# Optimization experiments

Hardware: AMD Instinct MI355X
Metric: run time of the kernel (lower is better)

The kernel has to match this reference:

```python
import jax, jax.numpy as jnp
import numpy as np

C = 128      # channels
ALPHA = 0.5
B, LX, LY = 8, 128, 1024


def setup_inputs() -> dict:
    key = jax.random.key(0)
    ks = jax.random.split(key, 10)
    s = 1.0 / np.sqrt(C)
    sh = 1.0 / np.sqrt(C // 2)
    return {
        "x": jax.random.normal(ks[0], (B, C, LX), dtype=jnp.float32),
        "y": jax.random.normal(ks[1], (B, C, LY), dtype=jnp.float32),
        "W_drug": jax.random.uniform(ks[2], (C, C), jnp.float32, -s, s),
        "b_drug": jax.random.uniform(ks[3], (C,), jnp.float32, -s, s),
        "W_prot": jax.random.uniform(ks[4], (C, C), jnp.float32, -s, s),
        "b_prot": jax.random.uniform(ks[5], (C,), jnp.float32, -s, s),
        "W_down": jax.random.uniform(ks[6], (C, C // 2), jnp.float32, -s, s),
        "b_down": jax.random.uniform(ks[7], (C // 2,), jnp.float32, -s, s),
        "W_up": jax.random.uniform(ks[8], (C // 2, C), jnp.float32, -sh, sh),
        "b_up": jax.random.uniform(ks[9], (C,), jnp.float32, -sh, sh),
    }


def reference(x, y, W_drug, b_drug, W_prot, b_prot, W_down, b_down, W_up, b_up):
    # x: [B, C, Lx], y: [B, C, Ly]
    drug_att = jnp.einsum("bcl,cd->bld", x, W_drug) + b_drug      # [B, Lx, C]
    prot_att = jnp.einsum("bcl,cd->bld", y, W_prot) + b_prot      # [B, Ly, C]
    # broadcast-add -> [B, Lx, Ly, C]
    s = jax.nn.relu(drug_att[:, :, None, :] + prot_att[:, None, :, :])
    h = jax.nn.relu(jnp.einsum("bxyc,ch->bxyh", s, W_down) + b_down)  # [B,Lx,Ly,C/2]
    atten = jnp.einsum("bxyh,hc->bxyc", h, W_up) + b_up              # [B,Lx,Ly,C]
    comp = jnp.mean(atten, axis=2)   # [B, Lx, C]
    prot = jnp.mean(atten, axis=1)   # [B, Ly, C]
    comp_g = comp.transpose(0, 2, 1)  # [B, C, Lx]
    prot_g = prot.transpose(0, 2, 1)  # [B, C, Ly]
    comp_gate = jax.nn.sigmoid(comp_g) * jnp.tanh(comp_g)
    prot_gate = jax.nn.sigmoid(prot_g) * jnp.tanh(prot_g)
    drug_out = x * ALPHA + x * comp_gate
    prot_out = y * ALPHA + y * prot_gate
    return (drug_out, prot_out)
```

## Files before the change

kernel.cpp:

```cpp
#include <hip/hip_runtime.h>
#include <hip/hip_bf16.h>
#include <math.h>

#define B_  8
#define C_  128
#define CH_ 64
#define LX_ 128
#define LY_ 1024

typedef __attribute__((ext_vector_type(8)))  _Float16 half8;
typedef __attribute__((ext_vector_type(16))) float f32x16;

__global__ __launch_bounds__(128) void k1_att(
    const float* __restrict__ x, const float* __restrict__ y,
    const float* __restrict__ Wd, const float* __restrict__ bd,
    const float* __restrict__ Wp, const float* __restrict__ bp,
    const float* __restrict__ Wdown,
    _Float16* __restrict__ datt, _Float16* __restrict__ patt,
    _Float16* __restrict__ wdTh)
{
    const int blk = blockIdx.x;
    const int t = threadIdx.x;
    if (blk < 64) {
        int u = blk * 128 + t;
        wdTh[u] = (_Float16)Wdown[(u & 127) * CH_ + (u >> 7)];
    }
    const float* src; const float* W; const float* bias; _Float16* dst; int L;
    int b, l0;
    if (blk < 256) {
        int row0 = blk * 4; b = row0 >> 7; l0 = row0 & 127;
        src = x; W = Wd; bias = bd; dst = datt; L = LX_;
    } else {
        int row0 = (blk - 256) * 4; b = row0 >> 10; l0 = row0 & 1023;
        src = y; W = Wp; bias = bp; dst = patt; L = LY_;
    }
    __shared__ float col[4][128];
    {
        const float* sp = src + ((long)b * C_ + t) * L + l0;
        float4 v = *(const float4*)sp;
        col[0][t] = v.x; col[1][t] = v.y; col[2][t] = v.z; col[3][t] = v.w;
    }
    __syncthreads();
    float acc0 = bias[t], acc1 = acc0, acc2 = acc0, acc3 = acc0;
    #pragma unroll 8
    for (int c = 0; c < 128; ++c) {
        float w = W[c * 128 + t];
        float s0 = col[0][c], s1 = col[1][c], s2 = col[2][c], s3 = col[3][c];
        acc0 = fmaf(s0, w, acc0); acc1 = fmaf(s1, w, acc1);
        acc2 = fmaf(s2, w, acc2); acc3 = fmaf(s3, w, acc3);
    }
    _Float16* dp = dst + ((long)b * L + l0) * C_ + t;
    dp[0]      = (_Float16)acc0; dp[C_]     = (_Float16)acc1;
    dp[2 * C_] = (_Float16)acc2; dp[3 * C_] = (_Float16)acc3;
}

__global__ __launch_bounds__(256, 3) void k2_main(
    const _Float16* __restrict__ datt, const _Float16* __restrict__ patt,
    const _Float16* __restrict__ wdTh, const float* __restrict__ bdown,
    float* __restrict__ HxP, float* __restrict__ HyP)
{
    const int b     = blockIdx.x >> 2;
    const int lxblk = blockIdx.x & 3;
    const int lyblk = blockIdx.y;
    const int t   = threadIdx.x;
    const int w   = t >> 6;
    const int wk  = w >> 1;
    const int wl  = w & 1;
    const int l   = t & 63;
    const int h   = l >> 5;
    const int c32 = l & 31;

    __shared__ float compWp[32][2][66];
    __shared__ float protP[2][32][66];

    const _Float16* prow = patt + ((long)(b * LY_) + lyblk * 32 + c32) * C_;
    const _Float16* wrow = wdTh + (wk * 32 + c32) * C_;
    half8 pv[8], bf[8];
    #pragma unroll
    for (int kt = 0; kt < 8; ++kt) {
        pv[kt] = *(const half8*)(prow + kt * 16 + h * 8);
        bf[kt] = *(const half8*)(wrow + kt * 16 + h * 8);
    }
    const float bdr = bdown[wk * 32 + c32];

    const _Float16* dbase = datt + ((long)(b * LX_) + lxblk * 32) * C_;
    const half8 hz = {};
    float hy[16];
    #pragma unroll
    for (int r = 0; r < 16; ++r) hy[r] = 0.f;

    #pragma unroll 1
    for (int lxp = 0; lxp < 8; ++lxp) {
        const int lxa = wl * 16 + lxp * 2;
        const _Float16* da = dbase + lxa * C_ + h * 8;
        f32x16 accA = {}, accB = {};
        #pragma unroll
        for (int kt = 0; kt < 8; ++kt) {
            half8 dva = *(const half8*)(da + kt * 16);
            half8 dvb = *(const half8*)(da + C_ + kt * 16);
            half8 sa = __builtin_elementwise_max(dva + pv[kt], hz);
            half8 sb = __builtin_elementwise_max(dvb + pv[kt], hz);
            accA = __builtin_amdgcn_mfma_f32_32x32x16_f16(sa, bf[kt], accA, 0, 0, 0);
            accB = __builtin_amdgcn_mfma_f32_32x32x16_f16(sb, bf[kt], accB, 0, 0, 0);
        }
        float sA = 0.f, sB = 0.f;
        #pragma unroll
        for (int r = 0; r < 16; ++r) {
            float va = fmaxf(accA[r] + bdr, 0.f);
            float vb = fmaxf(accB[r] + bdr, 0.f);
            hy[r] += va + vb;
            sA += va; sB += vb;
        }
        compWp[lxa][h][wk * 32 + c32]     = sA;
        compWp[lxa + 1][h][wk * 32 + c32] = sB;
    }

    #pragma unroll
    for (int r = 0; r < 16; ++r) {
        int ly = (r & 3) + 8 * (r >> 2) + 4 * h;
        protP[wl][ly][wk * 32 + c32] = hy[r];
    }
    __syncthreads();

    {
        float* hxp = HxP + ((long)lyblk * (B_ * LX_) + b * LX_ + lxblk * 32) * 64;
        float* hyp = HyP + ((long)lxblk * (B_ * LY_) + b * LY_ + lyblk * 32) * 64;
        for (int u = t; u < 2048; u += 256) {
            int r = u >> 6, c = u & 63;
            hxp[u] = compWp[r][0][c] + compWp[r][1][c];
            hyp[u] = protP[0][r][c] + protP[1][r][c];
        }
    }
}

__global__ __launch_bounds__(256) void k3_gate(
    const float* __restrict__ HxP, const float* __restrict__ HyP,
    const float* __restrict__ wup, const float* __restrict__ bup,
    const float* __restrict__ x, const float* __restrict__ y,
    float* __restrict__ out)
{
    const int b = blockIdx.y;
    const int t = threadIdx.x;
    const float* part; const float* xin; float* outp; int L; float invN; int l0;
    int nq; long qstr;
    if (blockIdx.x < 4) {
        part = HxP; nq = 32; qstr = (long)B_ * LX_ * 64;
        xin = x; outp = out; L = LX_; invN = 1.f / 1024.f; l0 = blockIdx.x * 32;
    } else {
        part = HyP; nq = 4;  qstr = (long)B_ * LY_ * 64;
        xin = y; outp = out + (long)B_ * C_ * LX_; L = LY_; invN = 1.f / 128.f;
        l0 = (blockIdx.x - 4) * 32;
    }
    __shared__ float Ht[32][72];
    __shared__ float Wt[64][136];
    __shared__ float gg[32][133];

    const float* p0 = part + ((long)b * L + l0) * 64;
    for (int u = t; u < 2048; u += 256) {
        float a0 = 0.f, a1 = 0.f, a2 = 0.f, a3 = 0.f;
        #pragma unroll 4
        for (int q = 0; q < nq; q += 4) {
            a0 += p0[(long)q * qstr + u];
            a1 += p0[(long)(q + 1) * qstr + u];
            a2 += p0[(long)(q + 2) * qstr + u];
            a3 += p0[(long)(q + 3) * qstr + u];
        }
        Ht[u >> 6][u & 63] = (a0 + a1) + (a2 + a3);
    }
    #pragma unroll
    for (int i = 0; i < 8; ++i) {
        int idx = t + i * 256;
        int r = idx >> 5, c4 = (idx & 31) * 4;
        *(float4*)&Wt[r][c4] = *(const float4*)(wup + idx * 4);
    }
    __syncthreads();

    const int lrow = t >> 3, cg = (t & 7) * 4;
    float acc[4][4];
    #pragma unroll
    for (int jj = 0; jj < 4; ++jj)
        #pragma unroll
        for (int i = 0; i < 4; ++i) acc[jj][i] = 0.f;
    #pragma unroll 4
    for (int k = 0; k < 64; ++k) {
        float hv = Ht[lrow][k];
        #pragma unroll
        for (int jj = 0; jj < 4; ++jj) {
            float4 wv = *(const float4*)&Wt[k][cg + 32 * jj];
            acc[jj][0] = fmaf(hv, wv.x, acc[jj][0]);
            acc[jj][1] = fmaf(hv, wv.y, acc[jj][1]);
            acc[jj][2] = fmaf(hv, wv.z, acc[jj][2]);
            acc[jj][3] = fmaf(hv, wv.w, acc[jj][3]);
        }
    }
    #pragma unroll
    for (int jj = 0; jj < 4; ++jj)
        #pragma unroll
        for (int i = 0; i < 4; ++i) {
            int c = cg + 32 * jj + i;
            float v = fmaf(acc[jj][i], invN, bup[c]);
            float sg = 1.f / (1.f + expf(-v));
            gg[lrow][c] = sg * tanhf(v);
        }
    __syncthreads();
    for (int u = t; u < 4096; u += 256) {
        int c = u >> 5, li = u & 31;
        long idx = ((long)b * C_ + c) * L + l0 + li;
        outp[idx] = xin[idx] * (0.5f + gg[li][c]);
    }
}

extern "C" void kernel_launch(void* const* d_in, const int* in_sizes, int n_in,
                              void* d_out, int out_size, void* d_ws, size_t ws_size,
                              hipStream_t stream) {
    (void)in_sizes; (void)n_in; (void)out_size; (void)ws_size;
    const float* x     = (const float*)d_in[0];
    const float* y     = (const float*)d_in[1];
    const float* Wdrug = (const float*)d_in[2];
    const float* bdrug = (const float*)d_in[3];
    const float* Wprot = (const float*)d_in[4];
    const float* bprot = (const float*)d_in[5];
    const float* Wdown = (const float*)d_in[6];
    const float* bdown = (const float*)d_in[7];
    const float* Wup   = (const float*)d_in[8];
    const float* bup   = (const float*)d_in[9];
    float* out = (float*)d_out;
    char* ws = (char*)d_ws;

    _Float16* datt = (_Float16*)ws;
    _Float16* patt = (_Float16*)(ws + 262144);
    _Float16* wdTh = (_Float16*)(ws + 2359296);
    float*    HxP  = (float*)(ws + 2375680);
    float*    HyP  = (float*)(ws + 10764288);

    hipLaunchKernelGGL(k1_att, dim3(2304), dim3(128), 0, stream,
                       x, y, Wdrug, bdrug, Wprot, bprot, Wdown, datt, patt, wdTh);
    hipLaunchKernelGGL(k2_main, dim3(32, 32, 1), dim3(256), 0, stream,
                       datt, patt, wdTh, bdown, HxP, HyP);
    hipLaunchKernelGGL(k3_gate, dim3(36, 8), dim3(256), 0, stream,
                       HxP, HyP, Wup, bup, x, y, out);
}
```

Measured before the change: 71.32 us.

## Loop each k2 block over four ly tiles and prefetch next drug rows

The main kernel's grid shrinks from 32x32 to 32x8 blocks, and each block now walks four ly tiles in sequence, reloading the protein rows per tile and keeping the down-projection weights in registers throughout. Inside the lx loop, the next pair of drug rows is loaded into registers before the MFMA chain runs, so global-load latency overlaps compute. The comp partial sums are also split into four independent accumulators to shorten the dependency chain. In exchange the kernel uses more registers, so launch bounds drop to two blocks per SM. It also adds an extra barrier per tile, and the smaller grid gives fewer blocks to balance across the 256 CUs.

```diff
diff --git a/kernel.cpp b/kernel.cpp
--- a/kernel.cpp
+++ b/kernel.cpp
@@ -54,14 +54,13 @@
     dp[2 * C_] = (_Float16)acc2; dp[3 * C_] = (_Float16)acc3;
 }
 
-__global__ __launch_bounds__(256, 3) void k2_main(
+__global__ __launch_bounds__(256, 2) void k2_main(
     const _Float16* __restrict__ datt, const _Float16* __restrict__ patt,
     const _Float16* __restrict__ wdTh, const float* __restrict__ bdown,
     float* __restrict__ HxP, float* __restrict__ HyP)
 {
     const int b     = blockIdx.x >> 2;
     const int lxblk = blockIdx.x & 3;
-    const int lyblk = blockIdx.y;
     const int t   = threadIdx.x;
     const int w   = t >> 6;
     const int wk  = w >> 1;
@@ -73,63 +72,88 @@
     __shared__ float compWp[32][2][66];
     __shared__ float protP[2][32][66];
 
-    const _Float16* prow = patt + ((long)(b * LY_) + lyblk * 32 + c32) * C_;
-    const _Float16* wrow = wdTh + (wk * 32 + c32) * C_;
-    half8 pv[8], bf[8];
-    #pragma unroll
-    for (int kt = 0; kt < 8; ++kt) {
-        pv[kt] = *(const half8*)(prow + kt * 16 + h * 8);
-        bf[kt] = *(const half8*)(wrow + kt * 16 + h * 8);
-    }
+    const _Float16* wrow = wdTh + (wk * 32 + c32) * C_ + h * 8;
+    half8 bf[8];
+    #pragma unroll
+    for (int kt = 0; kt < 8; ++kt) bf[kt] = *(const half8*)(wrow + kt * 16);
     const float bdr = bdown[wk * 32 + c32];
-
-    const _Float16* dbase = datt + ((long)(b * LX_) + lxblk * 32) * C_;
+    const _Float16* dbase =
+        datt + ((long)(b * LX_) + lxblk * 32 + wl * 16) * C_ + h * 8;
     const half8 hz = {};
-    float hy[16];
-    #pragma unroll
-    for (int r = 0; r < 16; ++r) hy[r] = 0.f;
 
     #pragma unroll 1
-    for (int lxp = 0; lxp < 8; ++lxp) {
-        const int lxa = wl * 16 + lxp * 2;
-        const _Float16* da = dbase + lxa * C_ + h * 8;
-        f32x16 accA = {}, accB = {};
+    for (int tt = 0; tt < 4; ++tt) {
+        const int lyblk = blockIdx.y * 4 + tt;
+        const _Float16* prow =
+            patt + ((long)(b * LY_) + lyblk * 32 + c32) * C_ + h * 8;
+        half8 pv[8];
+        #pragma unroll
+        for (int kt = 0; kt < 8; ++kt) pv[kt] = *(const half8*)(prow + kt * 16);
+
+        float hy[16];
+        #pragma unroll
+        for (int r = 0; r < 16; ++r) hy[r] = 0.f;
+
+        half8 dva[8], dvb[8];
         #pragma unroll
         for (int kt = 0; kt < 8; ++kt) {
-            half8 dva = *(const half8*)(da + kt * 16);
-            half8 dvb = *(const half8*)(da + C_ + kt * 16);
-            half8 sa = __builtin_elementwise_max(dva + pv[kt], hz);
-            half8 sb = __builtin_elementwise_max(dvb + pv[kt], hz);
-            accA = __builtin_amdgcn_mfma_f32_32x32x16_f16(sa, bf[kt], accA, 0, 0, 0);
-            accB = __builtin_amdgcn_mfma_f32_32x32x16_f16(sb, bf[kt], accB, 0, 0, 0);
-        }
-        float sA = 0.f, sB = 0.f;
+            dva[kt] = *(const half8*)(dbase + kt * 16);
+            dvb[kt] = *(const half8*)(dbase + C_ + kt * 16);
+        }
+
+        #pragma unroll 1
+        for (int lxp = 0; lxp < 8; ++lxp) {
+            half8 sa[8], sb[8];
+            #pragma unroll
+            for (int kt = 0; kt < 8; ++kt) {
+                sa[kt] = __builtin_elementwise_max(dva[kt] + pv[kt], hz);
+                sb[kt] = __builtin_elementwise_max(dvb[kt] + pv[kt], hz);
+            }
+            if (lxp < 7) {
+                const _Float16* dn = dbase + (lxp * 2 + 2) * C_;
+                #pragma unroll
+                for (int kt = 0; kt < 8; ++kt) {
+                    dva[kt] = *(const half8*)(dn + kt * 16);
+                    dvb[kt] = *(const half8*)(dn + C_ + kt * 16);
+                }
+            }
+            f32x16 accA = {}, accB = {};
+            #pragma unroll
+            for (int kt = 0; kt < 8; ++kt) {
+                accA = __builtin_amdgcn_mfma_f32_32x32x16_f16(sa[kt], bf[kt], accA, 0, 0, 0);
+                accB = __builtin_amdgcn_mfma_f32_32x32x16_f16(sb[kt], bf[kt], accB, 0, 0, 0);
+            }
+            const int lxa = wl * 16 + lxp * 2;
+            float pa[4] = {0.f, 0.f, 0.f, 0.f}, pb[4] = {0.f, 0.f, 0.f, 0.f};
+            #pragma unroll
+            for (int r = 0; r < 16; ++r) {
+                float va = fmaxf(accA[r] + bdr, 0.f);
+                float vb = fmaxf(accB[r] + bdr, 0.f);
+                hy[r] += va + vb;
+                pa[r & 3] += va;
+                pb[r & 3] += vb;
+            }
+            compWp[lxa][h][wk * 32 + c32]     = (pa[0] + pa[1]) + (pa[2] + pa[3]);
+            compWp[lxa + 1][h][wk * 32 + c32] = (pb[0] + pb[1]) + (pb[2] + pb[3]);
+        }
+
         #pragma unroll
         for (int r = 0; r < 16; ++r) {
-            float va = fmaxf(accA[r] + bdr, 0.f);
-            float vb = fmaxf(accB[r] + bdr, 0.f);
-            hy[r] += va + vb;
-            sA += va; sB += vb;
-        }
-        compWp[lxa][h][wk * 32 + c32]     = sA;
-        compWp[lxa + 1][h][wk * 32 + c32] = sB;
-    }
-
-    #pragma unroll
-    for (int r = 0; r < 16; ++r) {
-        int ly = (r & 3) + 8 * (r >> 2) + 4 * h;
-        protP[wl][ly][wk * 32 + c32] = hy[r];
-    }
-    __syncthreads();
-
-    {
-        float* hxp = HxP + ((long)lyblk * (B_ * LX_) + b * LX_ + lxblk * 32) * 64;
-        float* hyp = HyP + ((long)lxblk * (B_ * LY_) + b * LY_ + lyblk * 32) * 64;
-        for (int u = t; u < 2048; u += 256) {
-            int r = u >> 6, c = u & 63;
-            hxp[u] = compWp[r][0][c] + compWp[r][1][c];
-            hyp[u] = protP[0][r][c] + protP[1][r][c];
-        }
+            int ly = (r & 3) + 8 * (r >> 2) + 4 * h;
+            protP[wl][ly][wk * 32 + c32] = hy[r];
+        }
+        __syncthreads();
+
+        {
+            float* hxp = HxP + ((long)lyblk * (B_ * LX_) + b * LX_ + lxblk * 32) * 64;
+            float* hyp = HyP + ((long)lxblk * (B_ * LY_) + b * LY_ + lyblk * 32) * 64;
+            for (int u = t; u < 2048; u += 256) {
+                int r = u >> 6, c = u & 63;
+                hxp[u] = compWp[r][0][c] + compWp[r][1][c];
+                hyp[u] = protP[0][r][c] + protP[1][r][c];
+            }
+        }
+        __syncthreads();
     }
 }
 
@@ -235,7 +259,7 @@
 
     hipLaunchKernelGGL(k1_att, dim3(2304), dim3(128), 0, stream,
                        x, y, Wdrug, bdrug, Wprot, bprot, Wdown, datt, patt, wdTh);
-    hipLaunchKernelGGL(k2_main, dim3(32, 32, 1), dim3(256), 0, stream,
+    hipLaunchKernelGGL(k2_main, dim3(32, 8), dim3(256), 0, stream,
                        datt, patt, wdTh, bdown, HxP, HyP);
     hipLaunchKernelGGL(k3_gate, dim3(36, 8), dim3(256), 0, stream,
                        HxP, HyP, Wup, bup, x, y, out);
```

Measured after the change: 79.06 us. +10.9%, slower.

## Split k2 warps over lx rows, compute both hidden halves per warp with prefetch

Applied to the files above, without the earlier changes.

Each of the four warps in k2_main now owns 8 lx rows and computes both 32-column halves of the hidden layer. This lets one relu'd activation tile feed two MFMAs, so the add/max work on the operand is halved. The next row's datt fragment is double-buffered in registers so its global loads overlap the current MFMAs. The cost is higher register pressure (two weight fragment sets, two hy accumulators, two data buffers), handled by lowering the occupancy hint from 3 to 2 blocks, plus a larger protP shared buffer reduced over four warps.

```diff
diff --git a/kernel.cpp b/kernel.cpp
--- a/kernel.cpp
+++ b/kernel.cpp
@@ -54,7 +54,7 @@
     dp[2 * C_] = (_Float16)acc2; dp[3 * C_] = (_Float16)acc3;
 }
 
-__global__ __launch_bounds__(256, 3) void k2_main(
+__global__ __launch_bounds__(256, 2) void k2_main(
     const _Float16* __restrict__ datt, const _Float16* __restrict__ patt,
     const _Float16* __restrict__ wdTh, const float* __restrict__ bdown,
     float* __restrict__ HxP, float* __restrict__ HyP)
@@ -64,61 +64,82 @@
     const int lyblk = blockIdx.y;
     const int t   = threadIdx.x;
     const int w   = t >> 6;
-    const int wk  = w >> 1;
-    const int wl  = w & 1;
     const int l   = t & 63;
     const int h   = l >> 5;
     const int c32 = l & 31;
 
     __shared__ float compWp[32][2][66];
-    __shared__ float protP[2][32][66];
-
-    const _Float16* prow = patt + ((long)(b * LY_) + lyblk * 32 + c32) * C_;
-    const _Float16* wrow = wdTh + (wk * 32 + c32) * C_;
-    half8 pv[8], bf[8];
+    __shared__ float protP[4][32][66];
+
+    const _Float16* w0 = wdTh + c32 * C_ + h * 8;
+    const _Float16* w1 = wdTh + (32 + c32) * C_ + h * 8;
+    const _Float16* prow = patt + ((long)(b * LY_) + lyblk * 32 + c32) * C_ + h * 8;
+    half8 bf0[8], bf1[8], pv[8];
     #pragma unroll
     for (int kt = 0; kt < 8; ++kt) {
-        pv[kt] = *(const half8*)(prow + kt * 16 + h * 8);
-        bf[kt] = *(const half8*)(wrow + kt * 16 + h * 8);
-    }
-    const float bdr = bdown[wk * 32 + c32];
-
-    const _Float16* dbase = datt + ((long)(b * LX_) + lxblk * 32) * C_;
+        bf0[kt] = *(const half8*)(w0 + kt * 16);
+        bf1[kt] = *(const half8*)(w1 + kt * 16);
+        pv[kt]  = *(const half8*)(prow + kt * 16);
+    }
+    const float bdr0 = bdown[c32], bdr1 = bdown[32 + c32];
+
+    const _Float16* dbase =
+        datt + ((long)(b * LX_) + lxblk * 32 + w * 8) * C_ + h * 8;
     const half8 hz = {};
-    float hy[16];
-    #pragma unroll
-    for (int r = 0; r < 16; ++r) hy[r] = 0.f;
+    float hy0[16], hy1[16];
+    #pragma unroll
+    for (int r = 0; r < 16; ++r) { hy0[r] = 0.f; hy1[r] = 0.f; }
+
+    half8 dcA[8], dcB[8];
+    #pragma unroll
+    for (int kt = 0; kt < 8; ++kt)
+        dcA[kt] = *(const half8*)(dbase + kt * 16);
+
+#define K2_COMPUTE(ROW, DC)                                                   \
+    {                                                                         \
+        f32x16 acc0 = {}, acc1 = {};                                          \
+        _Pragma("unroll")                                                     \
+        for (int kt = 0; kt < 8; ++kt) {                                      \
+            half8 s = __builtin_elementwise_max(DC[kt] + pv[kt], hz);         \
+            acc0 = __builtin_amdgcn_mfma_f32_32x32x16_f16(s, bf0[kt], acc0, 0, 0, 0); \
+            acc1 = __builtin_amdgcn_mfma_f32_32x32x16_f16(s, bf1[kt], acc1, 0, 0, 0); \
+        }                                                                     \
+        float s0 = 0.f, s1 = 0.f;                                             \
+        _Pragma("unroll")                                                     \
+        for (int r = 0; r < 16; ++r) {                                        \
+            float va = fmaxf(acc0[r] + bdr0, 0.f);                            \
+            float vb = fmaxf(acc1[r] + bdr1, 0.f);                            \
+            hy0[r] += va; hy1[r] += vb;                                       \
+            s0 += va; s1 += vb;                                               \
+        }                                                                     \
+        const int lxi = w * 8 + (ROW);                                        \
+        compWp[lxi][h][c32]      = s0;                                        \
+        compWp[lxi][h][32 + c32] = s1;                                        \
+    }
 
     #pragma unroll 1
-    for (int lxp = 0; lxp < 8; ++lxp) {
-        const int lxa = wl * 16 + lxp * 2;
-        const _Float16* da = dbase + lxa * C_ + h * 8;
-        f32x16 accA = {}, accB = {};
-        #pragma unroll
-        for (int kt = 0; kt < 8; ++kt) {
-            half8 dva = *(const half8*)(da + kt * 16);
-            half8 dvb = *(const half8*)(da + C_ + kt * 16);
-            half8 sa = __builtin_elementwise_max(dva + pv[kt], hz);
-            half8 sb = __builtin_elementwise_max(dvb + pv[kt], hz);
-            accA = __builtin_amdgcn_mfma_f32_32x32x16_f16(sa, bf[kt], accA, 0, 0, 0);
-            accB = __builtin_amdgcn_mfma_f32_32x32x16_f16(sb, bf[kt], accB, 0, 0, 0);
-        }
-        float sA = 0.f, sB = 0.f;
-        #pragma unroll
-        for (int r = 0; r < 16; ++r) {
-            float va = fmaxf(accA[r] + bdr, 0.f);
-            float vb = fmaxf(accB[r] + bdr, 0.f);
-            hy[r] += va + vb;
-            sA += va; sB += vb;
-        }
-        compWp[lxa][h][wk * 32 + c32]     = sA;
-        compWp[lxa + 1][h][wk * 32 + c32] = sB;
-    }
+    for (int lxp = 0; lxp < 4; ++lxp) {
+        const int rA = lxp * 2, rB = rA + 1;
+        {
+            const _Float16* dp = dbase + rB * C_;
+            #pragma unroll
+            for (int kt = 0; kt < 8; ++kt) dcB[kt] = *(const half8*)(dp + kt * 16);
+        }
+        K2_COMPUTE(rA, dcA);
+        {
+            const _Float16* dp = dbase + ((rB + 1) & 7) * C_;
+            #pragma unroll
+            for (int kt = 0; kt < 8; ++kt) dcA[kt] = *(const half8*)(dp + kt * 16);
+        }
+        K2_COMPUTE(rB, dcB);
+    }
+#undef K2_COMPUTE
 
     #pragma unroll
     for (int r = 0; r < 16; ++r) {
         int ly = (r & 3) + 8 * (r >> 2) + 4 * h;
-        protP[wl][ly][wk * 32 + c32] = hy[r];
+        protP[w][ly][c32]      = hy0[r];
+        protP[w][ly][32 + c32] = hy1[r];
     }
     __syncthreads();
 
@@ -128,7 +149,8 @@
         for (int u = t; u < 2048; u += 256) {
             int r = u >> 6, c = u & 63;
             hxp[u] = compWp[r][0][c] + compWp[r][1][c];
-            hyp[u] = protP[0][r][c] + protP[1][r][c];
+            hyp[u] = (protP[0][r][c] + protP[1][r][c])
+                   + (protP[2][r][c] + protP[3][r][c]);
         }
     }
 }
@@ -235,7 +257,7 @@
 
     hipLaunchKernelGGL(k1_att, dim3(2304), dim3(128), 0, stream,
                        x, y, Wdrug, bdrug, Wprot, bprot, Wdown, datt, patt, wdTh);
-    hipLaunchKernelGGL(k2_main, dim3(32, 32, 1), dim3(256), 0, stream,
+    hipLaunchKernelGGL(k2_main, dim3(32, 32), dim3(256), 0, stream,
                        datt, patt, wdTh, bdown, HxP, HyP);
     hipLaunchKernelGGL(k3_gate, dim3(36, 8), dim3(256), 0, stream,
                        HxP, HyP, Wup, bup, x, y, out);
```

Result: faster. 65.70 us (-7.9%).

## Split main kernel into single-wave blocks with swizzled grid and partial HyP

Applied to the files above, without the earlier changes.

The main MFMA kernel moves from 256-thread blocks covering 32 lx rows to 64-thread single-wavefront blocks covering 16 lx rows and one half of the hidden channels. The block index is swizzled across batches. HyP partials are written straight from registers instead of going through shared memory. This creates 4096 small blocks to improve occupancy and load balance, but it doubles the number of HyP partial slices that the gate kernel must reduce (nq 4 to 8) and loses the two-row MFMA interleaving per wave.

```diff
diff --git a/kernel.cpp b/kernel.cpp
--- a/kernel.cpp
+++ b/kernel.cpp
@@ -54,81 +54,81 @@
     dp[2 * C_] = (_Float16)acc2; dp[3 * C_] = (_Float16)acc3;
 }
 
-__global__ __launch_bounds__(256, 3) void k2_main(
+__global__ __launch_bounds__(64, 4) void k2_main(
     const _Float16* __restrict__ datt, const _Float16* __restrict__ patt,
     const _Float16* __restrict__ wdTh, const float* __restrict__ bdown,
     float* __restrict__ HxP, float* __restrict__ HyP)
 {
-    const int b     = blockIdx.x >> 2;
-    const int lxblk = blockIdx.x & 3;
-    const int lyblk = blockIdx.y;
-    const int t   = threadIdx.x;
-    const int w   = t >> 6;
-    const int wk  = w >> 1;
-    const int wl  = w & 1;
-    const int l   = t & 63;
+    const int raw = blockIdx.x;
+    const int bid = (raw & 7) * 512 + (raw >> 3);
+    const int wk    = bid & 1;
+    const int lxg   = (bid >> 1) & 7;
+    const int lyblk = (bid >> 4) & 31;
+    const int b     = bid >> 9;
+    const int l   = threadIdx.x;
     const int h   = l >> 5;
     const int c32 = l & 31;
 
-    __shared__ float compWp[32][2][66];
-    __shared__ float protP[2][32][66];
-
-    const _Float16* prow = patt + ((long)(b * LY_) + lyblk * 32 + c32) * C_;
-    const _Float16* wrow = wdTh + (wk * 32 + c32) * C_;
+    __shared__ float HxL[16][2][32];
+
+    const _Float16* prow = patt + ((long)(b * LY_) + lyblk * 32 + c32) * C_ + h * 8;
+    const _Float16* wrow = wdTh + (wk * 32 + c32) * C_ + h * 8;
     half8 pv[8], bf[8];
     #pragma unroll
     for (int kt = 0; kt < 8; ++kt) {
-        pv[kt] = *(const half8*)(prow + kt * 16 + h * 8);
-        bf[kt] = *(const half8*)(wrow + kt * 16 + h * 8);
+        pv[kt] = *(const half8*)(prow + kt * 16);
+        bf[kt] = *(const half8*)(wrow + kt * 16);
     }
     const float bdr = bdown[wk * 32 + c32];
-
-    const _Float16* dbase = datt + ((long)(b * LX_) + lxblk * 32) * C_;
+    const f32x16 zero16 = {};
     const half8 hz = {};
+    const _Float16* dbase = datt + ((long)(b * LX_) + lxg * 16) * C_ + h * 8;
+
     float hy[16];
     #pragma unroll
     for (int r = 0; r < 16; ++r) hy[r] = 0.f;
 
     #pragma unroll 1
-    for (int lxp = 0; lxp < 8; ++lxp) {
-        const int lxa = wl * 16 + lxp * 2;
-        const _Float16* da = dbase + lxa * C_ + h * 8;
-        f32x16 accA = {}, accB = {};
-        #pragma unroll
-        for (int kt = 0; kt < 8; ++kt) {
-            half8 dva = *(const half8*)(da + kt * 16);
-            half8 dvb = *(const half8*)(da + C_ + kt * 16);
-            half8 sa = __builtin_elementwise_max(dva + pv[kt], hz);
-            half8 sb = __builtin_elementwise_max(dvb + pv[kt], hz);
-            accA = __builtin_amdgcn_mfma_f32_32x32x16_f16(sa, bf[kt], accA, 0, 0, 0);
-            accB = __builtin_amdgcn_mfma_f32_32x32x16_f16(sb, bf[kt], accB, 0, 0, 0);
-        }
-        float sA = 0.f, sB = 0.f;
-        #pragma unroll
-        for (int r = 0; r < 16; ++r) {
-            float va = fmaxf(accA[r] + bdr, 0.f);
-            float vb = fmaxf(accB[r] + bdr, 0.f);
-            hy[r] += va + vb;
-            sA += va; sB += vb;
-        }
-        compWp[lxa][h][wk * 32 + c32]     = sA;
-        compWp[lxa + 1][h][wk * 32 + c32] = sB;
-    }
-
-    #pragma unroll
     for (int r = 0; r < 16; ++r) {
-        int ly = (r & 3) + 8 * (r >> 2) + 4 * h;
-        protP[wl][ly][wk * 32 + c32] = hy[r];
-    }
-    __syncthreads();
+        const _Float16* dp = dbase + r * C_;
+        half8 s = __builtin_elementwise_max(*(const half8*)dp + pv[0], hz);
+        f32x16 acc =
+            __builtin_amdgcn_mfma_f32_32x32x16_f16(s, bf[0], zero16, 0, 0, 0);
+        #pragma unroll
+        for (int kt = 1; kt < 8; ++kt) {
+            half8 s2 =
+                __builtin_elementwise_max(*(const half8*)(dp + kt * 16) + pv[kt], hz);
+            acc = __builtin_amdgcn_mfma_f32_32x32x16_f16(s2, bf[kt], acc, 0, 0, 0);
+        }
+        float ssum = 0.f;
+        #pragma unroll
+        for (int rr = 0; rr < 16; ++rr) {
+            float v = fmaxf(acc[rr] + bdr, 0.f);
+            hy[rr] += v;
+            ssum += v;
+        }
+        HxL[r][h][c32] = ssum;
+    }
 
     {
-        float* hxp = HxP + ((long)lyblk * (B_ * LX_) + b * LX_ + lxblk * 32) * 64;
-        float* hyp = HyP + ((long)lxblk * (B_ * LY_) + b * LY_ + lyblk * 32) * 64;
-        for (int u = t; u < 2048; u += 256) {
-            int r = u >> 6, c = u & 63;
-            hxp[u] = compWp[r][0][c] + compWp[r][1][c];
-            hyp[u] = protP[0][r][c] + protP[1][r][c];
+        float* hyp = HyP + (((long)lxg * B_ + b) * LY_ + lyblk * 32) * 64
+                   + wk * 32 + c32;
+        #pragma unroll
+        for (int rr = 0; rr < 16; ++rr) {
+            int ly = (rr & 3) + 8 * (rr >> 2) + 4 * h;
+            hyp[(long)ly * 64] = hy[rr];
+        }
+    }
+
+    __syncthreads();
+
+    {
+        float* hxp = HxP + (((long)lyblk * B_ + b) * LX_ + lxg * 16) * 64
+                   + wk * 32 + c32;
+        #pragma unroll
+        for (int i = 0; i < 8; ++i) {
+            int r = h * 8 + i;
+            hxp[(long)r * 64] = HxL[r][0][c32] + HxL[r][1][c32];
         }
     }
 }
@@ -147,7 +147,7 @@
         part = HxP; nq = 32; qstr = (long)B_ * LX_ * 64;
         xin = x; outp = out; L = LX_; invN = 1.f / 1024.f; l0 = blockIdx.x * 32;
     } else {
-        part = HyP; nq = 4;  qstr = (long)B_ * LY_ * 64;
+        part = HyP; nq = 8;  qstr = (long)B_ * LY_ * 64;
         xin = y; outp = out + (long)B_ * C_ * LX_; L = LY_; invN = 1.f / 128.f;
         l0 = (blockIdx.x - 4) * 32;
     }
@@ -235,7 +235,7 @@
 
     hipLaunchKernelGGL(k1_att, dim3(2304), dim3(128), 0, stream,
                        x, y, Wdrug, bdrug, Wprot, bprot, Wdown, datt, patt, wdTh);
-    hipLaunchKernelGGL(k2_main, dim3(32, 32, 1), dim3(256), 0, stream,
+    hipLaunchKernelGGL(k2_main, dim3(4096), dim3(64), 0, stream,
                        datt, patt, wdTh, bdown, HxP, HyP);
     hipLaunchKernelGGL(k3_gate, dim3(36, 8), dim3(256), 0, stream,
                        HxP, HyP, Wup, bup, x, y, out);
```

After: 72.01 us. Within noise of the previous version (+1.0%).
